# Kernel tuning notes

Hardware: AMD Instinct MI355X
Metric: run time of the kernel (lower is better)

The kernel has to match this reference:

```python
import jax, jax.numpy as jnp
import numpy as np

E = 1024
H = 16
D = E // H
B = 32
S = 1024


def _layernorm(x, gamma, beta, eps=1e-5):
    mu = jnp.mean(x, axis=-1, keepdims=True)
    var = jnp.var(x, axis=-1, keepdims=True)
    return (x - mu) * jax.lax.rsqrt(var + eps) * gamma + beta


def setup_inputs() -> dict:
    key = jax.random.key(0)
    ks = jax.random.split(key, 16)
    w = lambda k, shape: jax.random.normal(k, shape, dtype=jnp.float32) * 0.02
    return {
        "img_feat": jax.random.normal(ks[0], (B, S, E), dtype=jnp.float32),
        "heat_feat": jax.random.normal(ks[1], (B, E), dtype=jnp.float32),
        "W_img": w(ks[2], (E, E)), "b_img": jnp.zeros((E,), jnp.float32),
        "W_heat": w(ks[3], (E, E)), "b_heat": jnp.zeros((E,), jnp.float32),
        "Wq": w(ks[4], (E, E)), "bq": jnp.zeros((E,), jnp.float32),
        "Wk": w(ks[5], (E, E)), "bk": jnp.zeros((E,), jnp.float32),
        "Wv": w(ks[6], (E, E)), "bv": jnp.zeros((E,), jnp.float32),
        "Wo": w(ks[7], (E, E)), "bo": jnp.zeros((E,), jnp.float32),
        "gamma": jnp.ones((E,), jnp.float32),
        "beta": jnp.zeros((E,), jnp.float32),
    }


def reference(img_feat, heat_feat, W_img, b_img, W_heat, b_heat,
              Wq, bq, Wk, bk, Wv, bv, Wo, bo, gamma, beta):
    # projections (torch Linear: x @ W.T + b)
    proj_heat = (heat_feat @ W_heat.T + b_heat)[:, None, :]        # [B,1,E]
    proj_img = img_feat @ W_img.T + b_img                          # [B,S,E]
    # multi-head attention, KV seq len = 1
    q = (proj_img @ Wq.T + bq).reshape(B, S, H, D)
    k = (proj_heat @ Wk.T + bk).reshape(B, 1, H, D)
    v = (proj_heat @ Wv.T + bv).reshape(B, 1, H, D)
    scale = 1.0 / np.sqrt(D).astype(np.float32)
    scores = jnp.einsum('bshd,bthd->bhst', q, k) * scale           # [B,H,S,1]
    attn = jax.nn.softmax(scores, axis=-1)                         # == ones
    ctx = jnp.einsum('bhst,bthd->bshd', attn, v).reshape(B, S, E)
    attn_out = ctx @ Wo.T + bo                                     # [B,S,E]
    # residual + LayerNorm (dropout is identity in eval)
    return _layernorm(img_feat + attn_out, gamma, beta)
```

## Files before the change

### kernel.cpp

```cpp
#include <hip/hip_runtime.h>


#define E_DIM 1024
#define B_DIM 32
#define S_DIM 1024

__global__ __launch_bounds__(256) void gemv_xlds(
        const float* __restrict__ W,
        const float* __restrict__ bias,
        const float* __restrict__ x,
        float* __restrict__ y) {
    __shared__ float4 xs[8 * 256];
    const int t = threadIdx.x;
    const int rg = blockIdx.x & 255;
    const int bq = blockIdx.x >> 8;

    const float4* x4 = reinterpret_cast<const float4*>(x) + (size_t)bq * 8 * 256;
    #pragma unroll
    for (int i = 0; i < 8; ++i)
        xs[i * 256 + t] = x4[i * 256 + t];
    __syncthreads();

    const int wave = t >> 6;
    const int lane = t & 63;
    const int e = rg * 4 + wave;

    const float4* w4 = reinterpret_cast<const float4*>(W + (size_t)e * E_DIM);
    float4 w0 = w4[lane];
    float4 w1 = w4[64 + lane];
    float4 w2 = w4[128 + lane];
    float4 w3 = w4[192 + lane];

    float acc[8];
    #pragma unroll
    for (int i = 0; i < 8; ++i) acc[i] = 0.f;

    #pragma unroll
    for (int i = 0; i < 8; ++i) {
        float4 a0 = xs[i * 256 + lane];
        float4 a1 = xs[i * 256 + 64 + lane];
        float4 a2 = xs[i * 256 + 128 + lane];
        float4 a3 = xs[i * 256 + 192 + lane];
        float r = w0.x * a0.x + w0.y * a0.y + w0.z * a0.z + w0.w * a0.w;
        r += w1.x * a1.x + w1.y * a1.y + w1.z * a1.z + w1.w * a1.w;
        r += w2.x * a2.x + w2.y * a2.y + w2.z * a2.z + w2.w * a2.w;
        r += w3.x * a3.x + w3.y * a3.y + w3.z * a3.z + w3.w * a3.w;
        acc[i] = r;
    }

    #pragma unroll
    for (int off = 32; off; off >>= 1) {
        #pragma unroll
        for (int i = 0; i < 8; ++i)
            acc[i] += __shfl_xor(acc[i], off, 64);
    }

    if (lane == 0) {
        const float bs = bias[e];
        #pragma unroll
        for (int i = 0; i < 8; ++i)
            y[(size_t)(bq * 8 + i) * E_DIM + e] = acc[i] + bs;
    }
}

__global__ __launch_bounds__(256) void resid_ln(
        const float* __restrict__ img,
        const float* __restrict__ a,
        const float* __restrict__ gamma,
        const float* __restrict__ beta,
        float* __restrict__ out) {
    const int t = threadIdx.x;
    const int wave = t >> 6;
    const int lane = t & 63;
    const int row0 = blockIdx.x * 32 + wave * 8;
    const int b = row0 >> 10;

    const float4* g4  = reinterpret_cast<const float4*>(gamma);
    const float4* be4 = reinterpret_cast<const float4*>(beta);
    const float4* a4  = reinterpret_cast<const float4*>(a + (size_t)b * E_DIM);
    float4 gv[4], bv[4], av[4];
    #pragma unroll
    for (int p = 0; p < 4; ++p) {
        gv[p] = g4[p * 64 + lane];
        bv[p] = be4[p * 64 + lane];
        av[p] = a4[p * 64 + lane];
    }

    float4 xA[4], xB[4], xC[4];

#define LN_LOAD(X, rr)                                                        \
    {                                                                         \
        const float4* i4 =                                                    \
            reinterpret_cast<const float4*>(img + (size_t)(row0 + (rr)) * E_DIM); \
        X[0] = i4[lane];                                                      \
        X[1] = i4[64 + lane];                                                 \
        X[2] = i4[128 + lane];                                                \
        X[3] = i4[192 + lane];                                                \
    }

#define LN_PROC(X, rr)                                                        \
    {                                                                         \
        float4 y[4];                                                          \
        float s = 0.f, q = 0.f;                                               \
        _Pragma("unroll")                                                     \
        for (int p = 0; p < 4; ++p) {                                         \
            y[p].x = X[p].x + av[p].x;                                        \
            y[p].y = X[p].y + av[p].y;                                        \
            y[p].z = X[p].z + av[p].z;                                        \
            y[p].w = X[p].w + av[p].w;                                        \
            s += y[p].x + y[p].y + y[p].z + y[p].w;                           \
            q += y[p].x * y[p].x + y[p].y * y[p].y                            \
               + y[p].z * y[p].z + y[p].w * y[p].w;                           \
        }                                                                     \
        _Pragma("unroll")                                                     \
        for (int off = 32; off; off >>= 1) {                                  \
            s += __shfl_xor(s, off, 64);                                      \
            q += __shfl_xor(q, off, 64);                                      \
        }                                                                     \
        const float mu   = s * (1.0f / E_DIM);                                \
        const float rstd = rsqrtf(q * (1.0f / E_DIM) - mu * mu + 1e-5f);      \
        float4* o4 =                                                          \
            reinterpret_cast<float4*>(out + (size_t)(row0 + (rr)) * E_DIM);   \
        _Pragma("unroll")                                                     \
        for (int p = 0; p < 4; ++p) {                                         \
            float4 ov;                                                        \
            ov.x = (y[p].x - mu) * rstd * gv[p].x + bv[p].x;                  \
            ov.y = (y[p].y - mu) * rstd * gv[p].y + bv[p].y;                  \
            ov.z = (y[p].z - mu) * rstd * gv[p].z + bv[p].z;                  \
            ov.w = (y[p].w - mu) * rstd * gv[p].w + bv[p].w;                  \
            o4[p * 64 + lane] = ov;                                           \
        }                                                                     \
    }

    LN_LOAD(xA, 0)
    LN_LOAD(xB, 1)
    LN_LOAD(xC, 2) LN_PROC(xA, 0)
    LN_LOAD(xA, 3) LN_PROC(xB, 1)
    LN_LOAD(xB, 4) LN_PROC(xC, 2)
    LN_LOAD(xC, 5) LN_PROC(xA, 3)
    LN_LOAD(xA, 6) LN_PROC(xB, 4)
    LN_LOAD(xB, 7) LN_PROC(xC, 5)
    LN_PROC(xA, 6)
    LN_PROC(xB, 7)

#undef LN_LOAD
#undef LN_PROC
}

extern "C" void kernel_launch(void* const* d_in, const int* in_sizes, int n_in,
                              void* d_out, int out_size, void* d_ws, size_t ws_size,
                              hipStream_t stream) {
    const float* heat   = (const float*)d_in[1];
    const float* W_heat = (const float*)d_in[4];
    const float* b_heat = (const float*)d_in[5];
    const float* Wv     = (const float*)d_in[10];
    const float* bvv    = (const float*)d_in[11];
    const float* Wo     = (const float*)d_in[12];
    const float* bo     = (const float*)d_in[13];
    const float* img    = (const float*)d_in[0];
    const float* gamma  = (const float*)d_in[14];
    const float* beta   = (const float*)d_in[15];
    float* out = (float*)d_out;

    float* ws = (float*)d_ws;
    float* tt = ws;
    float* vv = ws + B_DIM * E_DIM;
    float* aa = ws + 2 * B_DIM * E_DIM;

    gemv_xlds<<<1024, 256, 0, stream>>>(W_heat, b_heat, heat, tt);
    gemv_xlds<<<1024, 256, 0, stream>>>(Wv, bvv, tt, vv);
    gemv_xlds<<<1024, 256, 0, stream>>>(Wo, bo, vv, aa);

    resid_ln<<<(B_DIM * S_DIM) / 32, 256, 0, stream>>>(img, aa, gamma, beta, out);
}
```

Measured before the change: 289.9 us.

## Split residual LayerNorm into separate statistics and apply kernels

Replaces the fused residual+LayerNorm kernel with two kernels. The first computes per-row mean and rstd into a workspace buffer; the second is a flat elementwise kernel that rereads img and applies the normalization. The intent is simpler, more parallel access patterns in each pass, at the cost of reading the large img tensor twice plus an extra launch.

```diff
diff --git a/kernel.cpp b/kernel.cpp
--- a/kernel.cpp
+++ b/kernel.cpp
@@ -63,28 +63,20 @@
     }
 }
 
-__global__ __launch_bounds__(256) void resid_ln(
+__global__ __launch_bounds__(256) void ln_stats(
         const float* __restrict__ img,
         const float* __restrict__ a,
-        const float* __restrict__ gamma,
-        const float* __restrict__ beta,
-        float* __restrict__ out) {
+        float2* __restrict__ stats) {
     const int t = threadIdx.x;
     const int wave = t >> 6;
     const int lane = t & 63;
     const int row0 = blockIdx.x * 32 + wave * 8;
     const int b = row0 >> 10;
 
-    const float4* g4  = reinterpret_cast<const float4*>(gamma);
-    const float4* be4 = reinterpret_cast<const float4*>(beta);
-    const float4* a4  = reinterpret_cast<const float4*>(a + (size_t)b * E_DIM);
-    float4 gv[4], bv[4], av[4];
+    const float4* a4 = reinterpret_cast<const float4*>(a + (size_t)b * E_DIM);
+    float4 av[4];
     #pragma unroll
-    for (int p = 0; p < 4; ++p) {
-        gv[p] = g4[p * 64 + lane];
-        bv[p] = be4[p * 64 + lane];
-        av[p] = a4[p * 64 + lane];
-    }
+    for (int p = 0; p < 4; ++p) av[p] = a4[p * 64 + lane];
 
     float4 xA[4], xB[4], xC[4];
 
@@ -98,53 +90,81 @@
         X[3] = i4[192 + lane];                                                \
     }
 
-#define LN_PROC(X, rr)                                                        \
+#define LN_STAT(X, rr)                                                        \
     {                                                                         \
-        float4 y[4];                                                          \
         float s = 0.f, q = 0.f;                                               \
         _Pragma("unroll")                                                     \
         for (int p = 0; p < 4; ++p) {                                         \
-            y[p].x = X[p].x + av[p].x;                                        \
-            y[p].y = X[p].y + av[p].y;                                        \
-            y[p].z = X[p].z + av[p].z;                                        \
-            y[p].w = X[p].w + av[p].w;                                        \
-            s += y[p].x + y[p].y + y[p].z + y[p].w;                           \
-            q += y[p].x * y[p].x + y[p].y * y[p].y                            \
-               + y[p].z * y[p].z + y[p].w * y[p].w;                           \
+            float yx = X[p].x + av[p].x;                                      \
+            float yy = X[p].y + av[p].y;                                      \
+            float yz = X[p].z + av[p].z;                                      \
+            float yw = X[p].w + av[p].w;                                      \
+            s += yx + yy + yz + yw;                                           \
+            q += yx * yx + yy * yy + yz * yz + yw * yw;                       \
         }                                                                     \
         _Pragma("unroll")                                                     \
         for (int off = 32; off; off >>= 1) {                                  \
             s += __shfl_xor(s, off, 64);                                      \
             q += __shfl_xor(q, off, 64);                                      \
         }                                                                     \
-        const float mu   = s * (1.0f / E_DIM);                                \
-        const float rstd = rsqrtf(q * (1.0f / E_DIM) - mu * mu + 1e-5f);      \
-        float4* o4 =                                                          \
-            reinterpret_cast<float4*>(out + (size_t)(row0 + (rr)) * E_DIM);   \
-        _Pragma("unroll")                                                     \
-        for (int p = 0; p < 4; ++p) {                                         \
-            float4 ov;                                                        \
-            ov.x = (y[p].x - mu) * rstd * gv[p].x + bv[p].x;                  \
-            ov.y = (y[p].y - mu) * rstd * gv[p].y + bv[p].y;                  \
-            ov.z = (y[p].z - mu) * rstd * gv[p].z + bv[p].z;                  \
-            ov.w = (y[p].w - mu) * rstd * gv[p].w + bv[p].w;                  \
-            o4[p * 64 + lane] = ov;                                           \
+        if (lane == 0) {                                                      \
+            const float mu = s * (1.0f / E_DIM);                              \
+            float2 st;                                                        \
+            st.x = mu;                                                        \
+            st.y = rsqrtf(q * (1.0f / E_DIM) - mu * mu + 1e-5f);              \
+            stats[row0 + (rr)] = st;                                          \
         }                                                                     \
     }
 
     LN_LOAD(xA, 0)
     LN_LOAD(xB, 1)
-    LN_LOAD(xC, 2) LN_PROC(xA, 0)
-    LN_LOAD(xA, 3) LN_PROC(xB, 1)
-    LN_LOAD(xB, 4) LN_PROC(xC, 2)
-    LN_LOAD(xC, 5) LN_PROC(xA, 3)
-    LN_LOAD(xA, 6) LN_PROC(xB, 4)
-    LN_LOAD(xB, 7) LN_PROC(xC, 5)
-    LN_PROC(xA, 6)
-    LN_PROC(xB, 7)
+    LN_LOAD(xC, 2) LN_STAT(xA, 0)
+    LN_LOAD(xA, 3) LN_STAT(xB, 1)
+    LN_LOAD(xB, 4) LN_STAT(xC, 2)
+    LN_LOAD(xC, 5) LN_STAT(xA, 3)
+    LN_LOAD(xA, 6) LN_STAT(xB, 4)
+    LN_LOAD(xB, 7) LN_STAT(xC, 5)
+    LN_STAT(xA, 6)
+    LN_STAT(xB, 7)
 
 #undef LN_LOAD
-#undef LN_PROC
+#undef LN_STAT
+}
+
+__global__ __launch_bounds__(256) void ln_apply(
+        const float* __restrict__ img,
+        const float* __restrict__ a,
+        const float* __restrict__ gamma,
+        const float* __restrict__ beta,
+        const float2* __restrict__ stats,
+        float* __restrict__ out) {
+    const int tid = blockIdx.x * 256 + threadIdx.x;
+    const float4* img4 = reinterpret_cast<const float4*>(img);
+    const float4* a4   = reinterpret_cast<const float4*>(a);
+    const float4* g4   = reinterpret_cast<const float4*>(gamma);
+    const float4* b4   = reinterpret_cast<const float4*>(beta);
+    float4* out4 = reinterpret_cast<float4*>(out);
+
+    #pragma unroll 4
+    for (int k = 0; k < 16; ++k) {
+        const int i = tid + k * 524288;
+        const int row = i >> 8;
+        const int e4 = i & 255;
+        const int b = row >> 10;
+
+        float4 iv = img4[i];
+        float4 av = a4[b * 256 + e4];
+        float2 st = stats[row];
+        float4 gv = g4[e4];
+        float4 bv = b4[e4];
+
+        float4 ov;
+        ov.x = (iv.x + av.x - st.x) * st.y * gv.x + bv.x;
+        ov.y = (iv.y + av.y - st.x) * st.y * gv.y + bv.y;
+        ov.z = (iv.z + av.z - st.x) * st.y * gv.z + bv.z;
+        ov.w = (iv.w + av.w - st.x) * st.y * gv.w + bv.w;
+        out4[i] = ov;
+    }
 }
 
 extern "C" void kernel_launch(void* const* d_in, const int* in_sizes, int n_in,
@@ -166,10 +186,12 @@
     float* tt = ws;
     float* vv = ws + B_DIM * E_DIM;
     float* aa = ws + 2 * B_DIM * E_DIM;
+    float2* st = (float2*)(ws + 3 * B_DIM * E_DIM);
 
     gemv_xlds<<<1024, 256, 0, stream>>>(W_heat, b_heat, heat, tt);
     gemv_xlds<<<1024, 256, 0, stream>>>(Wv, bvv, tt, vv);
     gemv_xlds<<<1024, 256, 0, stream>>>(Wo, bo, vv, aa);
 
-    resid_ln<<<(B_DIM * S_DIM) / 32, 256, 0, stream>>>(img, aa, gamma, beta, out);
+    ln_stats<<<(B_DIM * S_DIM) / 32, 256, 0, stream>>>(img, aa, st);
+    ln_apply<<<2048, 256, 0, stream>>>(img, aa, gamma, beta, st, out);
 }
```

Result: slower. 309.7 us (+6.8%).
